# Kernel tuning notes

Hardware: AMD Instinct MI355X
Metric: run time of the kernel (lower is better)

The kernel has to match this reference:

```python
import jax, jax.numpy as jnp
import numpy as np

K = 512       # num_embeddings
D = 64        # dim_embeddings
BETA = 0.25   # commit_gain
GAMMA = 0.99  # EMA decay
EPS = 1e-05   # Laplace smoothing


def setup_inputs() -> dict:
    key = jax.random.key(0)
    k1, k2, k3 = jax.random.split(key, 3)
    enc_pred = jax.random.normal(k1, (32, D, 64, 64), dtype=jnp.float32)
    embeddings = jax.random.normal(k2, (K, D), dtype=jnp.float32)
    ema_m = jax.random.normal(k3, (K, D), dtype=jnp.float32)
    ema_M = jnp.zeros((K, 1), dtype=jnp.float32)
    return {"enc_pred": enc_pred, "embeddings": embeddings,
            "ema_m": ema_m, "ema_M": ema_M}


def reference(enc_pred, embeddings, ema_m, ema_M):
    B, _, H, W = enc_pred.shape
    x = jnp.transpose(enc_pred, (0, 2, 3, 1))          # [B, H, W, D]
    flat = x.reshape(-1, D)                            # [N, D], N = B*H*W

    # Squared L2 distances to all codewords: [N, K]
    dist = (jnp.sum(flat * flat, axis=1, keepdims=True)
            + jnp.sum(embeddings * embeddings, axis=1)
            - 2.0 * flat @ embeddings.T)
    idx = jnp.argmin(dist, axis=1)                     # [N]

    # Codebook lookup (equivalent to one-hot @ embeddings)
    quantized = embeddings[idx].reshape(x.shape)       # [B, H, W, D]

    # EMA codebook update (training branch, no_grad in torch)
    dm = jax.ops.segment_sum(flat, idx, num_segments=K)                 # [K, D]
    counts = jax.ops.segment_sum(jnp.ones((flat.shape[0], 1), flat.dtype),
                                 idx, num_segments=K)                   # [K, 1]
    new_m = GAMMA * ema_m + (1.0 - GAMMA) * dm
    new_M = GAMMA * ema_M + (1.0 - GAMMA) * counts
    N_tot = jnp.sum(new_M)
    new_M = (new_M + EPS) / (N_tot + EPS * K) * N_tot
    new_embeddings = new_m / new_M

    # Commitment loss (quantized detached)
    loss = BETA * jnp.mean((jax.lax.stop_gradient(quantized) - x) ** 2)

    # Straight-through estimator
    quant_ste = x + jax.lax.stop_gradient(quantized - x)
    out = jnp.transpose(quant_ste, (0, 3, 1, 2))       # [B, D, H, W]

    idx_ret = idx.reshape(B, H, W)[:, None, :, :]      # [B, 1, H, W]
    return (out, loss, idx_ret, new_embeddings, new_m, new_M)
```

## Files before the change

### kernel.cpp

```cpp
#include <hip/hip_runtime.h>

#define KCODES 512
#define DIM 64
#define NB 32
#define NH 64
#define NW 64
#define NPTS (NB*NH*NW)
#define HW (NH*NW)

#define O_OUT  0
#define O_LOSS 8388608
#define O_IDX  8388609
#define O_EMB  8519681
#define O_M    8552449
#define O_MM   8585217

#define W_DM   0
#define W_CNT  (KCODES*DIM)
#define W_LOSS (W_CNT + KCODES)
#define W_C    (W_LOSS + 1)
#define W_NEWM (W_C + KCODES)
#define W_TOTAL (W_NEWM + KCODES)

#define XPAD 68
#define EPAD 68

__global__ void cnorm_kernel(const float* __restrict__ emb, float* __restrict__ ws) {
    int k = blockIdx.x * blockDim.x + threadIdx.x;
    if (k >= KCODES) return;
    float s = 0.f;
    #pragma unroll
    for (int d = 0; d < DIM; ++d) { float v = emb[k*DIM + d]; s += v*v; }
    ws[W_C + k] = s;
}

__global__ __launch_bounds__(256, 2) void assign_kernel(
    const float* __restrict__ enc, const float* __restrict__ emb,
    float* __restrict__ out, float* __restrict__ ws)
{
    __shared__ float XL[128*XPAD];
    __shared__ float EL[128*EPAD];
    __shared__ float cnT[128];
    __shared__ int   bestI[128];

    const int t  = threadIdx.x;
    const int tx = t & 15;
    const int ty = t >> 4;

    const int R0 = blockIdx.x * 2;
    #pragma unroll
    for (int r2 = 0; r2 < 2; ++r2) {
        int R = R0 + r2, b = R >> 6, h = R & 63;
        const float* base = enc + ((size_t)b*64)*HW + (size_t)h*64;
        #pragma unroll
        for (int it = 0; it < 4; ++it) {
            int d = it*16 + ty;
            float4 v = *(const float4*)(base + (size_t)d*HW + tx*4);
            int p0 = r2*64 + tx*4;
            XL[(p0+0)*XPAD + d] = v.x;
            XL[(p0+1)*XPAD + d] = v.y;
            XL[(p0+2)*XPAD + d] = v.z;
            XL[(p0+3)*XPAD + d] = v.w;
        }
    }

    float best[8]; int bidx[8];
    #pragma unroll
    for (int i = 0; i < 8; ++i) { best[i] = 3.402823466e38f; bidx[i] = 0; }

    for (int tile = 0; tile < 4; ++tile) {
        __syncthreads();
        const float* esrc = emb + (size_t)tile*128*64;
        #pragma unroll
        for (int it = 0; it < 8; ++it) {
            int idx = t + it*256;
            int row = idx >> 4;
            int col = (idx & 15)*4;
            float4 v = *(const float4*)(esrc + row*64 + col);
            *(float4*)(&EL[row*EPAD + col]) = v;
        }
        if (t < 128) cnT[t] = ws[W_C + tile*128 + t];
        __syncthreads();

        float acc[8][8];
        #pragma unroll
        for (int i = 0; i < 8; ++i)
            #pragma unroll
            for (int j = 0; j < 8; ++j) acc[i][j] = 0.f;

        for (int c = 0; c < 16; ++c) {
            float4 xf[8], ef[8];
            #pragma unroll
            for (int i = 0; i < 8; ++i) {
                int p = 2*ty + (i&1) + 32*(i>>1);
                xf[i] = *(const float4*)(&XL[p*XPAD + c*4]);
            }
            #pragma unroll
            for (int j = 0; j < 8; ++j) {
                int r = tx + 16*j;
                ef[j] = *(const float4*)(&EL[r*EPAD + c*4]);
            }
            #pragma unroll
            for (int i = 0; i < 8; ++i)
                #pragma unroll
                for (int j = 0; j < 8; ++j) {
                    acc[i][j] = fmaf(xf[i].x, ef[j].x, acc[i][j]);
                    acc[i][j] = fmaf(xf[i].y, ef[j].y, acc[i][j]);
                    acc[i][j] = fmaf(xf[i].z, ef[j].z, acc[i][j]);
                    acc[i][j] = fmaf(xf[i].w, ef[j].w, acc[i][j]);
                }
        }

        #pragma unroll
        for (int j = 0; j < 8; ++j) {
            int k = tile*128 + tx + 16*j;
            float cn = cnT[tx + 16*j];
            #pragma unroll
            for (int i = 0; i < 8; ++i) {
                float s = cn - 2.f*acc[i][j];
                if (s < best[i] || (s == best[i] && k < bidx[i])) { best[i] = s; bidx[i] = k; }
            }
        }
    }

    #pragma unroll
    for (int i = 0; i < 8; ++i) {
        float b = best[i]; int kx = bidx[i];
        #pragma unroll
        for (int off = 1; off < 16; off <<= 1) {
            float ob = __shfl_xor(b, off, 64);
            int   ok = __shfl_xor(kx, off, 64);
            if (ob < b || (ob == b && ok < kx)) { b = ob; kx = ok; }
        }
        if (tx == 0) bestI[2*ty + (i&1) + 32*(i>>1)] = kx;
    }
    __syncthreads();

    if (t < 128) out[O_IDX + (size_t)R0*64 + t] = (float)bestI[t];

    float (*T2)[64][17] = (float(*)[64][17])EL;
    const int wv = t >> 6, w = t & 63;
    const int row = wv & 1, dhalf = wv >> 1;
    const int pg = w >> 4, dl = w & 15;
    const int R = R0 + row, bb = R >> 6, hh = R & 63;
    float* po = out + O_OUT + ((size_t)bb*64)*HW + (size_t)hh*64 + w;
    float lsum = 0.f;

    #pragma unroll
    for (int c2 = 0; c2 < 2; ++c2) {
        int c = dhalf*2 + c2;
        #pragma unroll
        for (int jj = 0; jj < 16; ++jj) {
            int p16 = jj*4 + pg;
            int kb = bestI[row*64 + p16];
            T2[wv][p16][dl] = emb[kb*64 + c*16 + dl];
        }
        #pragma unroll
        for (int i = 0; i < 16; ++i) {
            int d = c*16 + i;
            float q = T2[wv][w][i];
            po[(size_t)d*HW] = q;
            float df = q - XL[(row*64 + w)*XPAD + d];
            lsum = fmaf(df, df, lsum);
        }
    }
    #pragma unroll
    for (int off = 32; off >= 1; off >>= 1) lsum += __shfl_down(lsum, off, 64);
    if (w == 0) atomicAdd(&ws[W_LOSS], lsum);
}

__global__ __launch_bounds__(256, 1) void scatter_kernel(
    const float* __restrict__ enc, const float* __restrict__ out,
    float* __restrict__ ws)
{
    __shared__ float dmL[KCODES][65];
    __shared__ float cntL[KCODES];
    __shared__ float T[4][64][17];
    const int t = threadIdx.x;
    const int w = t & 63;
    const int wv = t >> 6;
    const int pg = w >> 4, dl = w & 15;

    float* dmf = &dmL[0][0];
    for (int i = t; i < KCODES*65; i += 256) dmf[i] = 0.f;
    for (int i = t; i < KCODES; i += 256) cntL[i] = 0.f;
    __syncthreads();

    for (int r = 0; r < 2; ++r) {
        const int R = blockIdx.x * 8 + r*4 + wv;
        const int b = R >> 6, h = R & 63;
        const float* px = enc + (size_t)b * DIM * HW + (size_t)h * NW + w;
        int bidx = (int)out[O_IDX + (size_t)R*64 + w];
        atomicAdd(&cntL[bidx], 1.0f);

        #pragma unroll
        for (int c = 0; c < 4; ++c) {
            #pragma unroll
            for (int i = 0; i < 16; ++i)
                T[wv][w][i] = px[(size_t)(c*16 + i) * HW];
            #pragma unroll
            for (int jj = 0; jj < 16; ++jj) {
                int p = jj*4 + pg;
                int kb = __shfl(bidx, p, 64);
                atomicAdd(&dmL[kb][c*16 + dl], T[wv][p][dl]);
            }
        }
    }
    __syncthreads();

    for (int k = wv*128; k < wv*128 + 128; ++k) {
        float c = cntL[k];
        if (c == 0.f) continue;
        atomicAdd(&ws[W_DM + k*64 + w], dmL[k][w]);
        if (w == 0) atomicAdd(&ws[W_CNT + k], c);
    }
}

__global__ void finalizeA(const float* __restrict__ emaM,
                          float* __restrict__ out, float* __restrict__ ws)
{
    __shared__ float red[512];
    int k = threadIdx.x;
    float nM = 0.99f * emaM[k] + 0.01f * ws[W_CNT + k];
    red[k] = nM;
    __syncthreads();
    for (int s = 256; s >= 1; s >>= 1) {
        if (k < s) red[k] += red[k + s];
        __syncthreads();
    }
    float Ntot = red[0];
    float sm = (nM + 1e-5f) / (Ntot + 1e-5f * (float)KCODES) * Ntot;
    ws[W_NEWM + k] = sm;
    out[O_MM + k] = sm;
    if (k == 0) out[O_LOSS] = 0.25f * ws[W_LOSS] / (float)((size_t)NPTS * DIM);
}

__global__ void finalizeB(const float* __restrict__ emam,
                          float* __restrict__ out, const float* __restrict__ ws)
{
    int i = blockIdx.x * blockDim.x + threadIdx.x;
    int k = i >> 6;
    float nm = 0.99f * emam[i] + 0.01f * ws[W_DM + i];
    out[O_M + i] = nm;
    out[O_EMB + i] = nm / ws[W_NEWM + k];
}

extern "C" void kernel_launch(void* const* d_in, const int* in_sizes, int n_in,
                              void* d_out, int out_size, void* d_ws, size_t ws_size,
                              hipStream_t stream)
{
    const float* enc  = (const float*)d_in[0];
    const float* emb  = (const float*)d_in[1];
    const float* emam = (const float*)d_in[2];
    const float* emaM = (const float*)d_in[3];
    float* out = (float*)d_out;
    float* ws  = (float*)d_ws;

    hipMemsetAsync(ws, 0, (size_t)W_TOTAL * sizeof(float), stream);
    cnorm_kernel<<<2, 256, 0, stream>>>(emb, ws);
    assign_kernel<<<NPTS/128, 256, 0, stream>>>(enc, emb, out, ws);
    scatter_kernel<<<256, 256, 0, stream>>>(enc, out, ws);
    finalizeA<<<1, 512, 0, stream>>>(emaM, out, ws);
    finalizeB<<<(KCODES*DIM)/256, 256, 0, stream>>>(emam, out, ws);
}
```

Before: 277.2 us.

## Prefetch codebook tiles into registers and derive loss from min distance

The assign kernel now prefetches the next 128-code embedding tile into registers while the current tile is being processed. It also changes how the enc tile is loaded into LDS so that each thread writes a float4 along D. The commitment loss is now computed as the min distance plus each point's squared norm, accumulated through LDS atomics, which removes the per-element difference pass in the output loop. The cost is extra registers (eight float4 prefetch values) on top of a large accumulator array, which may lower occupancy. The loss formula can also differ slightly numerically from the direct squared difference.

```diff
diff --git a/kernel.cpp b/kernel.cpp
--- a/kernel.cpp
+++ b/kernel.cpp
@@ -42,25 +42,40 @@
     __shared__ float EL[128*EPAD];
     __shared__ float cnT[128];
     __shared__ int   bestI[128];
+    __shared__ float xxL[128];
 
     const int t  = threadIdx.x;
     const int tx = t & 15;
     const int ty = t >> 4;
-
+    const int wv = t >> 6, w = t & 63;
     const int R0 = blockIdx.x * 2;
+
+    if (t < 128) xxL[t] = 0.f;
+    __syncthreads();
+
     #pragma unroll
     for (int r2 = 0; r2 < 2; ++r2) {
         int R = R0 + r2, b = R >> 6, h = R & 63;
-        const float* base = enc + ((size_t)b*64)*HW + (size_t)h*64;
+        const float* base = enc + (size_t)b*64*HW + (size_t)h*64 + w;
+        int p = r2*64 + w;
         #pragma unroll
         for (int it = 0; it < 4; ++it) {
-            int d = it*16 + ty;
-            float4 v = *(const float4*)(base + (size_t)d*HW + tx*4);
-            int p0 = r2*64 + tx*4;
-            XL[(p0+0)*XPAD + d] = v.x;
-            XL[(p0+1)*XPAD + d] = v.y;
-            XL[(p0+2)*XPAD + d] = v.z;
-            XL[(p0+3)*XPAD + d] = v.w;
+            int q4 = it*4 + wv;
+            int d0 = q4*4;
+            float4 v = make_float4(base[(size_t)(d0+0)*HW], base[(size_t)(d0+1)*HW],
+                                   base[(size_t)(d0+2)*HW], base[(size_t)(d0+3)*HW]);
+            *(float4*)(&XL[p*XPAD + d0]) = v;
+            atomicAdd(&xxL[p], v.x*v.x + v.y*v.y + v.z*v.z + v.w*v.w);
+        }
+    }
+
+    float4 pre[8];
+    {
+        const float* esrc = emb;
+        #pragma unroll
+        for (int it = 0; it < 8; ++it) {
+            int idx = t + it*256;
+            pre[it] = *(const float4*)(esrc + (idx >> 4)*64 + (idx & 15)*4);
         }
     }
 
@@ -70,16 +85,20 @@
 
     for (int tile = 0; tile < 4; ++tile) {
         __syncthreads();
-        const float* esrc = emb + (size_t)tile*128*64;
         #pragma unroll
         for (int it = 0; it < 8; ++it) {
             int idx = t + it*256;
-            int row = idx >> 4;
-            int col = (idx & 15)*4;
-            float4 v = *(const float4*)(esrc + row*64 + col);
-            *(float4*)(&EL[row*EPAD + col]) = v;
+            *(float4*)(&EL[(idx >> 4)*EPAD + (idx & 15)*4]) = pre[it];
         }
         if (t < 128) cnT[t] = ws[W_C + tile*128 + t];
+        if (tile < 3) {
+            const float* esrc = emb + (size_t)(tile+1)*128*64;
+            #pragma unroll
+            for (int it = 0; it < 8; ++it) {
+                int idx = t + it*256;
+                pre[it] = *(const float4*)(esrc + (idx >> 4)*64 + (idx & 15)*4);
+            }
+        }
         __syncthreads();
 
         float acc[8][8];
@@ -123,6 +142,7 @@
         }
     }
 
+    float lsum = 0.f;
     #pragma unroll
     for (int i = 0; i < 8; ++i) {
         float b = best[i]; int kx = bidx[i];
@@ -132,19 +152,18 @@
             int   ok = __shfl_xor(kx, off, 64);
             if (ob < b || (ob == b && ok < kx)) { b = ob; kx = ok; }
         }
-        if (tx == 0) bestI[2*ty + (i&1) + 32*(i>>1)] = kx;
+        int p = 2*ty + (i&1) + 32*(i>>1);
+        if (tx == 0) { bestI[p] = kx; lsum += b + xxL[p]; }
     }
     __syncthreads();
 
     if (t < 128) out[O_IDX + (size_t)R0*64 + t] = (float)bestI[t];
 
     float (*T2)[64][17] = (float(*)[64][17])EL;
-    const int wv = t >> 6, w = t & 63;
     const int row = wv & 1, dhalf = wv >> 1;
     const int pg = w >> 4, dl = w & 15;
     const int R = R0 + row, bb = R >> 6, hh = R & 63;
     float* po = out + O_OUT + ((size_t)bb*64)*HW + (size_t)hh*64 + w;
-    float lsum = 0.f;
 
     #pragma unroll
     for (int c2 = 0; c2 < 2; ++c2) {
@@ -156,14 +175,10 @@
             T2[wv][p16][dl] = emb[kb*64 + c*16 + dl];
         }
         #pragma unroll
-        for (int i = 0; i < 16; ++i) {
-            int d = c*16 + i;
-            float q = T2[wv][w][i];
-            po[(size_t)d*HW] = q;
-            float df = q - XL[(row*64 + w)*XPAD + d];
-            lsum = fmaf(df, df, lsum);
-        }
-    }
+        for (int i = 0; i < 16; ++i)
+            po[(size_t)(c*16 + i)*HW] = T2[wv][w][i];
+    }
+
     #pragma unroll
     for (int off = 32; off >= 1; off >>= 1) lsum += __shfl_down(lsum, off, 64);
     if (w == 0) atomicAdd(&ws[W_LOSS], lsum);
```

New measurement: 285.7 us. +3.1%, slower.

## Move quantized output write and loss into scatter kernel, reshape loads

Applied to the files above, without the earlier changes.

The codebook gather, output write and commitment-loss accumulation move from the assign kernel into the scatter kernel. There, each element of the encoder input is read once and used both for the shared-memory dm accumulation and for the loss. The scatter kernel now runs 512 threads per block and processes 8 rows in one pass. The assign kernel's X load changes to per-lane scalar loads packed into float4 LDS stores. The workspace layout is reordered so the memset still covers everything. This rebalances work between the two kernels and drops the assign kernel's transpose staging. The trade-off is strided per-lane global reads and writes in scatter, with fewer waves in flight.

```diff
diff --git a/kernel.cpp b/kernel.cpp
--- a/kernel.cpp
+++ b/kernel.cpp
@@ -18,9 +18,9 @@
 #define W_DM   0
 #define W_CNT  (KCODES*DIM)
 #define W_LOSS (W_CNT + KCODES)
-#define W_C    (W_LOSS + 1)
-#define W_NEWM (W_C + KCODES)
-#define W_TOTAL (W_NEWM + KCODES)
+#define W_NEWM (W_LOSS + 1)
+#define W_C    (W_NEWM + KCODES)
+#define W_TOTAL (W_C + KCODES)
 
 #define XPAD 68
 #define EPAD 68
@@ -46,21 +46,20 @@
     const int t  = threadIdx.x;
     const int tx = t & 15;
     const int ty = t >> 4;
-
+    const int wv = t >> 6, w = t & 63;
     const int R0 = blockIdx.x * 2;
+
     #pragma unroll
     for (int r2 = 0; r2 < 2; ++r2) {
         int R = R0 + r2, b = R >> 6, h = R & 63;
-        const float* base = enc + ((size_t)b*64)*HW + (size_t)h*64;
+        const float* base = enc + (size_t)b*64*HW + (size_t)h*64 + w;
+        int p = r2*64 + w;
         #pragma unroll
         for (int it = 0; it < 4; ++it) {
-            int d = it*16 + ty;
-            float4 v = *(const float4*)(base + (size_t)d*HW + tx*4);
-            int p0 = r2*64 + tx*4;
-            XL[(p0+0)*XPAD + d] = v.x;
-            XL[(p0+1)*XPAD + d] = v.y;
-            XL[(p0+2)*XPAD + d] = v.z;
-            XL[(p0+3)*XPAD + d] = v.w;
+            int d0 = (it*4 + wv)*4;
+            float4 v = make_float4(base[(size_t)(d0+0)*HW], base[(size_t)(d0+1)*HW],
+                                   base[(size_t)(d0+2)*HW], base[(size_t)(d0+3)*HW]);
+            *(float4*)(&XL[p*XPAD + d0]) = v;
         }
     }
 
@@ -74,10 +73,8 @@
         #pragma unroll
         for (int it = 0; it < 8; ++it) {
             int idx = t + it*256;
-            int row = idx >> 4;
-            int col = (idx & 15)*4;
-            float4 v = *(const float4*)(esrc + row*64 + col);
-            *(float4*)(&EL[row*EPAD + col]) = v;
+            *(float4*)(&EL[(idx >> 4)*EPAD + (idx & 15)*4]) =
+                *(const float4*)(esrc + (idx >> 4)*64 + (idx & 15)*4);
         }
         if (t < 128) cnT[t] = ws[W_C + tile*128 + t];
         __syncthreads();
@@ -135,80 +132,64 @@
         if (tx == 0) bestI[2*ty + (i&1) + 32*(i>>1)] = kx;
     }
     __syncthreads();
-
     if (t < 128) out[O_IDX + (size_t)R0*64 + t] = (float)bestI[t];
-
-    float (*T2)[64][17] = (float(*)[64][17])EL;
-    const int wv = t >> 6, w = t & 63;
-    const int row = wv & 1, dhalf = wv >> 1;
-    const int pg = w >> 4, dl = w & 15;
-    const int R = R0 + row, bb = R >> 6, hh = R & 63;
-    float* po = out + O_OUT + ((size_t)bb*64)*HW + (size_t)hh*64 + w;
-    float lsum = 0.f;
-
-    #pragma unroll
-    for (int c2 = 0; c2 < 2; ++c2) {
-        int c = dhalf*2 + c2;
-        #pragma unroll
-        for (int jj = 0; jj < 16; ++jj) {
-            int p16 = jj*4 + pg;
-            int kb = bestI[row*64 + p16];
-            T2[wv][p16][dl] = emb[kb*64 + c*16 + dl];
-        }
-        #pragma unroll
-        for (int i = 0; i < 16; ++i) {
-            int d = c*16 + i;
-            float q = T2[wv][w][i];
-            po[(size_t)d*HW] = q;
-            float df = q - XL[(row*64 + w)*XPAD + d];
-            lsum = fmaf(df, df, lsum);
-        }
-    }
-    #pragma unroll
-    for (int off = 32; off >= 1; off >>= 1) lsum += __shfl_down(lsum, off, 64);
-    if (w == 0) atomicAdd(&ws[W_LOSS], lsum);
-}
-
-__global__ __launch_bounds__(256, 1) void scatter_kernel(
-    const float* __restrict__ enc, const float* __restrict__ out,
-    float* __restrict__ ws)
-{
-    __shared__ float dmL[KCODES][65];
+}
+
+__global__ __launch_bounds__(512, 1) void scatter_kernel(
+    const float* __restrict__ enc, const float* __restrict__ emb,
+    float* __restrict__ out, float* __restrict__ ws)
+{
+    __shared__ float dmL[KCODES][DIM+1];
     __shared__ float cntL[KCODES];
-    __shared__ float T[4][64][17];
-    const int t = threadIdx.x;
-    const int w = t & 63;
+    __shared__ float redL[8];
+
+    const int t  = threadIdx.x;
+    const int w  = t & 63;
     const int wv = t >> 6;
     const int pg = w >> 4, dl = w & 15;
 
     float* dmf = &dmL[0][0];
-    for (int i = t; i < KCODES*65; i += 256) dmf[i] = 0.f;
-    for (int i = t; i < KCODES; i += 256) cntL[i] = 0.f;
-    __syncthreads();
-
-    for (int r = 0; r < 2; ++r) {
-        const int R = blockIdx.x * 8 + r*4 + wv;
-        const int b = R >> 6, h = R & 63;
-        const float* px = enc + (size_t)b * DIM * HW + (size_t)h * NW + w;
-        int bidx = (int)out[O_IDX + (size_t)R*64 + w];
-        atomicAdd(&cntL[bidx], 1.0f);
-
-        #pragma unroll
-        for (int c = 0; c < 4; ++c) {
-            #pragma unroll
-            for (int i = 0; i < 16; ++i)
-                T[wv][w][i] = px[(size_t)(c*16 + i) * HW];
-            #pragma unroll
-            for (int jj = 0; jj < 16; ++jj) {
-                int p = jj*4 + pg;
-                int kb = __shfl(bidx, p, 64);
-                atomicAdd(&dmL[kb][c*16 + dl], T[wv][p][dl]);
-            }
-        }
-    }
-    __syncthreads();
-
-    for (int k = wv*128; k < wv*128 + 128; ++k) {
+    for (int i = t; i < KCODES*(DIM+1); i += 512) dmf[i] = 0.f;
+    if (t < KCODES) cntL[t] = 0.f;
+    __syncthreads();
+
+    const int R = blockIdx.x * 8 + wv;
+    const int b = R >> 6, h = R & 63;
+    const float* base  = enc + (size_t)b*(64*HW) + (size_t)h*64;
+    float*       obase = out + O_OUT + (size_t)b*(64*HW) + (size_t)h*64;
+
+    const int bidx = (int)out[O_IDX + (size_t)R*64 + w];
+    atomicAdd(&cntL[bidx], 1.0f);
+    float lsum = 0.f;
+
+    #pragma unroll
+    for (int c = 0; c < 4; ++c) {
+        #pragma unroll
+        for (int jj = 0; jj < 16; ++jj) {
+            int p  = jj*4 + pg;
+            int kb = __shfl(bidx, p, 64);
+            int d  = c*16 + dl;
+            float xv = base[(size_t)d*HW + p];
+            atomicAdd(&dmL[kb][d], xv);
+            float q = emb[kb*64 + d];
+            obase[(size_t)d*HW + p] = q;
+            float df = q - xv;
+            lsum = fmaf(df, df, lsum);
+        }
+    }
+
+    #pragma unroll
+    for (int off = 32; off >= 1; off >>= 1) lsum += __shfl_down(lsum, off, 64);
+    if (w == 0) redL[wv] = lsum;
+    __syncthreads();
+    if (t == 0) {
+        float s = 0.f;
+        #pragma unroll
+        for (int v = 0; v < 8; ++v) s += redL[v];
+        atomicAdd(&ws[W_LOSS], s);
+    }
+
+    for (int k = wv*64; k < wv*64 + 64; ++k) {
         float c = cntL[k];
         if (c == 0.f) continue;
         atomicAdd(&ws[W_DM + k*64 + w], dmL[k][w]);
@@ -259,7 +240,7 @@
     hipMemsetAsync(ws, 0, (size_t)W_TOTAL * sizeof(float), stream);
     cnorm_kernel<<<2, 256, 0, stream>>>(emb, ws);
     assign_kernel<<<NPTS/128, 256, 0, stream>>>(enc, emb, out, ws);
-    scatter_kernel<<<256, 256, 0, stream>>>(enc, out, ws);
+    scatter_kernel<<<256, 512, 0, stream>>>(enc, emb, out, ws);
     finalizeA<<<1, 512, 0, stream>>>(emaM, out, ws);
     finalizeB<<<(KCODES*DIM)/256, 256, 0, stream>>>(emam, out, ws);
 }
```

Measured after the change: 243.5 us. -12.2%, faster.
